# Optimization experiments

Measured on AMD Instinct MI355X. Metric: run time of the kernel, lower is better.

## Reference

```python
import jax, jax.numpy as jnp
import numpy as np

N_HEAD = 12


def setup_inputs() -> dict:
    key = jax.random.key(0)
    k1, k2, k3 = jax.random.split(key, 3)
    B, S, D = 4, 2048, 768
    x = jax.random.normal(k1, (B, S, D), dtype=jnp.float32)
    std = 0.02
    w_attn = jax.random.normal(k2, (D, 3 * D), dtype=jnp.float32) * std
    b_attn = jnp.zeros((3 * D,), dtype=jnp.float32)
    w_proj = jax.random.normal(k3, (D, D), dtype=jnp.float32) * std
    b_proj = jnp.zeros((D,), dtype=jnp.float32)
    return {"x": x, "w_attn": w_attn, "b_attn": b_attn,
            "w_proj": w_proj, "b_proj": b_proj}


def reference(x, w_attn, b_attn, w_proj, b_proj):
    B, S, D = x.shape
    H = N_HEAD
    hd = D // H
    # c_attn: [B,S,3D]
    qkv = jnp.einsum('bsd,de->bse', x, w_attn) + b_attn
    q, k, v = jnp.split(qkv, 3, axis=2)
    # split heads -> [B,H,S,hd]
    q = q.reshape(B, S, H, hd).transpose(0, 2, 1, 3)
    k = k.reshape(B, S, H, hd).transpose(0, 2, 1, 3)
    v = v.reshape(B, S, H, hd).transpose(0, 2, 1, 3)
    # scores [B,H,S,S]; scale=False in original default
    w = jnp.einsum('bhqd,bhkd->bhqk', q, k)
    # original mask trick: w*b + 1e-9*(1-b), b = lower-triangular ones
    mask = jnp.tril(jnp.ones((S, S), dtype=w.dtype))
    w = w * mask + 1e-9 * (1 - mask)
    w = jax.nn.softmax(w, axis=-1)
    a = jnp.einsum('bhqk,bhkd->bhqd', w, v)
    # merge heads -> [B,S,D]
    a = a.transpose(0, 2, 1, 3).reshape(B, S, D)
    # c_proj
    out = jnp.einsum('bsd,de->bse', a, w_proj) + b_proj
    return out
```

## Files before the change

kernel.cpp:

```cpp
#include <hip/hip_runtime.h>
#include <cstdint>

typedef unsigned short u16;
typedef __bf16 bf16;
typedef bf16 bf16x8 __attribute__((ext_vector_type(8)));
typedef u16 u16x4 __attribute__((ext_vector_type(4)));
typedef u16 u16x8 __attribute__((ext_vector_type(8)));
typedef float f32x4 __attribute__((ext_vector_type(4)));

__device__ __forceinline__ u16 f2b(float f) {
    return __builtin_bit_cast(u16, (bf16)f);
}
__device__ __forceinline__ float b2f(u16 u) {
    return __uint_as_float(((unsigned)u) << 16);
}
__device__ __forceinline__ float ex2(float x) {
#if __has_builtin(__builtin_amdgcn_exp2f)
    return __builtin_amdgcn_exp2f(x);
#else
    return exp2f(x);
#endif
}
__device__ __forceinline__ void load_lds16(const void* g, void* l) {
    auto gp = reinterpret_cast<const __attribute__((address_space(1))) void*>(
        reinterpret_cast<uintptr_t>(g));
    auto lp = reinterpret_cast<__attribute__((address_space(3))) void*>(
        reinterpret_cast<uintptr_t>(l));
    __builtin_amdgcn_global_load_lds(gp, lp, 16, 0, 0);
}
__device__ __forceinline__ f32x4 mfma16(bf16x8 a, bf16x8 b, f32x4 c) {
    return __builtin_amdgcn_mfma_f32_16x16x32_bf16(a, b, c, 0, 0, 0);
}

#define LOG2E 1.44269504088896340736f

__global__ __launch_bounds__(256) void prep_kernel(const float* __restrict__ x,
                                                   u16* __restrict__ xb,
                                                   const float* __restrict__ wa,
                                                   const float* __restrict__ wp,
                                                   u16* __restrict__ wTa,
                                                   u16* __restrict__ wTp) {
    __shared__ float tile[32][33];
    const int bx = blockIdx.x;
    if (bx < 2048) {
        const int n4 = 8192 * 768 / 4;
        int i = bx * 256 + threadIdx.x;
        for (; i < n4; i += 2048 * 256) {
            float4 v = ((const float4*)x)[i];
            u16x4 r;
            r[0] = f2b(v.x); r[1] = f2b(v.y); r[2] = f2b(v.z); r[3] = f2b(v.w);
            *(u16x4*)&xb[(size_t)i * 4] = r;
        }
        return;
    }
    const int idx = bx - 2048;
    const int nx = idx % 96, ky = idx / 96;
    const float* w;
    u16* wT;
    int N, n0;
    if (nx < 72) { w = wa; wT = wTa; N = 2304; n0 = nx * 32; }
    else         { w = wp; wT = wTp; N = 768;  n0 = (nx - 72) * 32; }
    const int K = 768, k0 = ky * 32;
    const int tx = threadIdx.x & 31, ty = threadIdx.x >> 5;
#pragma unroll
    for (int i = 0; i < 4; ++i)
        tile[ty + i * 8][tx] = w[(size_t)(k0 + ty + i * 8) * N + n0 + tx];
    __syncthreads();
#pragma unroll
    for (int i = 0; i < 4; ++i)
        wT[(size_t)(n0 + ty + i * 8) * K + k0 + tx] = f2b(tile[tx][ty + i * 8]);
}

template <int MODE>
__global__ __launch_bounds__(256, 2) void gemm_kernel(const u16* __restrict__ A,
                                                      const u16* __restrict__ Bt,
                                                      const float* __restrict__ bias,
                                                      void* __restrict__ out,
                                                      u16* __restrict__ vt,
                                                      float* __restrict__ ts_raw,
                                                      int M, int N, int K) {
    __shared__ __align__(16) u16 SMEM[4 * 128 * 64];
    const int tid = threadIdx.x;
    const int wave = tid >> 6, lane = tid & 63;
    const int l15 = lane & 15, lg = lane >> 4;
    const int gx = gridDim.x;
    const int nwg = gx * gridDim.y;
    const int lin = blockIdx.y * gx + blockIdx.x;
    const int swz = (lin & 7) * (nwg >> 3) + (lin >> 3);
    const int tm = (swz / gx) * 128, tn = (swz % gx) * 128;
    const int wr = (wave >> 1) * 64, wc = (wave & 1) * 64;

    f32x4 acc[4][4] = {};

    const int rbase = wave * 8 + (lane >> 3);
    const int sslot = (lane & 7) ^ (rbase & 7);
    const u16* gA = A + (size_t)(tm + rbase) * K + sslot * 8;
    const u16* gB = Bt + (size_t)(tn + rbase) * K + sslot * 8;
    const int woff = wave * 8 * 64;
    const int nkt = K >> 6;

#pragma unroll
    for (int i = 0; i < 4; ++i) {
        load_lds16(gA + (size_t)i * 32 * K, SMEM + woff + i * 32 * 64);
        load_lds16(gB + (size_t)i * 32 * K, SMEM + 8192 + woff + i * 32 * 64);
    }

    for (int kt = 0; kt < nkt; ++kt) {
        __syncthreads();
        const int cur = kt & 1;
        if (kt + 1 < nkt) {
            u16* ldsA = SMEM + (cur ^ 1) * 2 * 8192 + woff;
            u16* ldsB = ldsA + 8192;
#pragma unroll
            for (int i = 0; i < 4; ++i) {
                load_lds16(gA + (size_t)i * 32 * K + (kt + 1) * 64, ldsA + i * 32 * 64);
                load_lds16(gB + (size_t)i * 32 * K + (kt + 1) * 64, ldsB + i * 32 * 64);
            }
        }
        const u16* As = SMEM + cur * 2 * 8192;
        const u16* Bs = As + 8192;
#pragma unroll
        for (int kk = 0; kk < 64; kk += 32) {
            const int sb = kk >> 3;
            bf16x8 af[4], bfr[4];
#pragma unroll
            for (int m = 0; m < 4; ++m) {
                int row = wr + m * 16 + l15;
                af[m] = *(const bf16x8*)&As[row * 64 + (((sb + lg) ^ (row & 7))) * 8];
            }
#pragma unroll
            for (int n = 0; n < 4; ++n) {
                int row = wc + n * 16 + l15;
                bfr[n] = *(const bf16x8*)&Bs[row * 64 + (((sb + lg) ^ (row & 7))) * 8];
            }
#pragma unroll
            for (int m = 0; m < 4; ++m)
#pragma unroll
                for (int n = 0; n < 4; ++n)
                    acc[m][n] = mfma16(bfr[n], af[m], acc[m][n]);
        }
    }

    if (MODE == 1 && tn >= 1536) {
        const int b = tm >> 11;
        const int s0 = (tm & 2047) + wr;
        const int st = s0 >> 6;
        const int hh = (tn + wc - 1536) >> 6;
        const int bh = b * 12 + hh;
        f32x4 colsum[4] = {};
#pragma unroll
        for (int m = 0; m < 4; ++m) {
            const int s = s0 + m * 16 + l15;
#pragma unroll
            for (int n = 0; n < 4; ++n) {
                const int col = tn + wc + n * 16 + lg * 4;
                f32x4 v = acc[m][n] + *(const f32x4*)&bias[col];
                colsum[n] += v;
                const int dl = n * 16 + lg * 4;
#pragma unroll
                for (int r = 0; r < 4; ++r)
                    vt[((size_t)bh * 64 + dl + r) * 2048 + s] = f2b(v[r]);
            }
        }
#pragma unroll
        for (int n = 0; n < 4; ++n)
#pragma unroll
            for (int off = 1; off < 16; off <<= 1) {
                colsum[n][0] += __shfl_xor(colsum[n][0], off);
                colsum[n][1] += __shfl_xor(colsum[n][1], off);
                colsum[n][2] += __shfl_xor(colsum[n][2], off);
                colsum[n][3] += __shfl_xor(colsum[n][3], off);
            }
        if (l15 == 0) {
#pragma unroll
            for (int n = 0; n < 4; ++n)
                *(f32x4*)&ts_raw[((size_t)bh * 32 + st) * 64 + n * 16 + lg * 4] =
                    colsum[n];
        }
        return;
    }

    const float sc = (MODE == 1 && tn < 768) ? LOG2E : 1.f;
#pragma unroll
    for (int m = 0; m < 4; ++m) {
        const size_t row = (size_t)(tm + wr + m * 16 + l15);
#pragma unroll
        for (int n = 0; n < 4; ++n) {
            const int col = tn + wc + n * 16 + lg * 4;
            f32x4 v = (acc[m][n] + *(const f32x4*)&bias[col]) * sc;
            if constexpr (MODE == 1) {
                u16x4 pk;
#pragma unroll
                for (int r = 0; r < 4; ++r) pk[r] = f2b(v[r]);
                *(u16x4*)&((u16*)out)[row * N + col] = pk;
            } else {
                *(f32x4*)&((float*)out)[row * N + col] = v;
            }
        }
    }
}

__global__ __launch_bounds__(256, 5) void attn_kernel(const u16* __restrict__ qkv,
                                                      const u16* __restrict__ vt,
                                                      const float* __restrict__ ts_raw,
                                                      u16* __restrict__ aout) {
    __shared__ __align__(16) u16 Ks[2][64 * 64];
    __shared__ __align__(16) u16 Vs[2][64 * 64];
    const int bh = blockIdx.x;
    const int qt = 31 - blockIdx.y;
    const int b = bh / 12, h = bh % 12;
    const int tid = threadIdx.x, wave = tid >> 6, lane = tid & 63;
    const int l15 = lane & 15, lg = lane >> 4;
    const int q0 = qt * 64 + wave * 16;
    const size_t rowbase = (size_t)b * 2048;
    const float MASKVAL = 1e-9f * LOG2E;
    const float THR2 = 8.0f * LOG2E;

    bf16x8 qf[2];
#pragma unroll
    for (int ks = 0; ks < 2; ++ks)
        qf[ks] = *(const bf16x8*)(qkv + (rowbase + q0 + l15) * 2304 + h * 64 +
                                  ks * 32 + lg * 8);

    f32x4 o[4] = {};
    float mrun = -1e30f;
    f32x4 lacc = {};

    const int rbase = wave * 8 + (lane >> 3);
    const int sslot = (lane & 7) ^ (rbase & 7);
    const int sig0 = ((rbase & 0x1C) << 1) | (rbase & 3);
    const u16* gK = qkv + (rowbase + sig0) * 2304 + 768 + h * 64 + sslot * 8;
    const u16* gV = vt + ((size_t)bh * 64 + rbase) * 2048 + sslot * 8;
    const int ldsoff = wave * 8 * 64;
    u16* sK0 = &Ks[0][ldsoff];
    u16* sK1 = &Ks[1][ldsoff];
    u16* sV0 = &Vs[0][ldsoff];
    u16* sV1 = &Vs[1][ldsoff];
    const int xk0 = ((0 + lg) ^ (l15 & 7)) * 8;
    const int xk1 = ((4 + lg) ^ (l15 & 7)) * 8;

#define STAGE_PAIR(Kd, Vd, kp, vp)                       \
    load_lds16(kp, Kd);                                  \
    load_lds16(kp + (size_t)4 * 2304, Kd + 32 * 64);     \
    load_lds16(vp, Vd);                                  \
    load_lds16(vp + (size_t)32 * 2048, Vd + 32 * 64);

    auto process = [&](const u16* Kb, const u16* Vb, int kt) {
        f32x4 sacc[4] = {};
        __builtin_amdgcn_s_setprio(1);
#pragma unroll
        for (int n = 0; n < 4; ++n) {
            const int ra = (n * 16 + l15) * 64;
            sacc[n] = mfma16(*(const bf16x8*)&Kb[ra + xk0], qf[0], sacc[n]);
            sacc[n] = mfma16(*(const bf16x8*)&Kb[ra + xk1], qf[1], sacc[n]);
        }
        __builtin_amdgcn_s_setprio(0);

        if (kt == qt) {
            const int q = q0 + l15;
            const int kb = kt * 64 + lg * 8;
#pragma unroll
            for (int n = 0; n < 4; ++n) {
                const int kn = kb + (n & 1) * 32 + ((n >> 1) << 2);
#pragma unroll
                for (int r = 0; r < 4; ++r)
                    if (kn + r > q) sacc[n][r] = MASKVAL;
            }
        }

        float mx = fmaxf(fmaxf(sacc[0][0], sacc[0][1]), fmaxf(sacc[0][2], sacc[0][3]));
#pragma unroll
        for (int n = 1; n < 4; ++n)
            mx = fmaxf(mx, fmaxf(fmaxf(sacc[n][0], sacc[n][1]),
                                 fmaxf(sacc[n][2], sacc[n][3])));
        if (__any(mx > mrun + THR2)) {
            float rm = fmaxf(mx, __shfl_xor(mx, 16));
            rm = fmaxf(rm, __shfl_xor(rm, 32));
            const float mnew = fmaxf(mrun, rm);
            const float alpha = ex2(mrun - mnew);
            mrun = mnew;
            lacc *= alpha;
#pragma unroll
            for (int dn = 0; dn < 4; ++dn) o[dn] *= alpha;
        }

#pragma unroll
        for (int n = 0; n < 4; ++n)
#pragma unroll
            for (int r = 0; r < 4; ++r)
                sacc[n][r] = ex2(sacc[n][r] - mrun);
        lacc += (sacc[0] + sacc[1]) + (sacc[2] + sacc[3]);

        bf16x8 bp0, bp1;
#pragma unroll
        for (int j = 0; j < 4; ++j) {
            bp0[j]     = (bf16)sacc[0][j];
            bp0[j + 4] = (bf16)sacc[2][j];
            bp1[j]     = (bf16)sacc[1][j];
            bp1[j + 4] = (bf16)sacc[3][j];
        }

        __builtin_amdgcn_s_setprio(1);
#pragma unroll
        for (int dn = 0; dn < 4; ++dn) {
            const int ra = (dn * 16 + l15) * 64;
            o[dn] = mfma16(*(const bf16x8*)&Vb[ra + xk0], bp0, o[dn]);
            o[dn] = mfma16(*(const bf16x8*)&Vb[ra + xk1], bp1, o[dn]);
        }
        __builtin_amdgcn_s_setprio(0);
    };

    const int nkt = qt + 1;
    STAGE_PAIR(sK0, sV0, gK, gV);
    const u16* gKp = gK + (size_t)64 * 2304;
    const u16* gVp = gV + 64;

    int kt = 0;
    for (;;) {
        __syncthreads();
        if (kt + 1 < nkt) {
            STAGE_PAIR(sK1, sV1, gKp, gVp);
            gKp += (size_t)64 * 2304; gVp += 64;
        }
        process(Ks[0], Vs[0], kt);
        if (++kt == nkt) break;
        __syncthreads();
        if (kt + 1 < nkt) {
            STAGE_PAIR(sK0, sV0, gKp, gVp);
            gKp += (size_t)64 * 2304; gVp += 64;
        }
        process(Ks[1], Vs[1], kt);
        if (++kt == nkt) break;
    }
#undef STAGE_PAIR

    float lrun = (lacc[0] + lacc[1]) + (lacc[2] + lacc[3]);
    lrun += __shfl_xor(lrun, 16);
    lrun += __shfl_xor(lrun, 32);

    if (qt < 31) {
        const float nf = (float)((31 - qt) * 64);
        const float mnew = fmaxf(mrun, MASKVAL);
        const float a = ex2(mrun - mnew);
        const float c = ex2(MASKVAL - mnew);
        lrun = lrun * a + nf * c;
        f32x4 suf[4] = {};
        for (int t = qt + 1; t < 32; ++t) {
            const float* sp = ts_raw + ((size_t)bh * 32 + t) * 64;
#pragma unroll
            for (int dn = 0; dn < 4; ++dn)
                suf[dn] += *(const f32x4*)&sp[dn * 16 + lg * 4];
        }
#pragma unroll
        for (int dn = 0; dn < 4; ++dn)
            o[dn] = o[dn] * a + suf[dn] * c;
    }

    const float inv = 1.f / lrun;
    const size_t row = rowbase + q0 + l15;
#pragma unroll
    for (int dn = 0; dn < 4; ++dn) {
        u16x4 st;
#pragma unroll
        for (int r = 0; r < 4; ++r) st[r] = f2b(o[dn][r] * inv);
        *(u16x4*)&aout[row * 768 + h * 64 + dn * 16 + lg * 4] = st;
    }
}

extern "C" void kernel_launch(void* const* d_in, const int* in_sizes, int n_in,
                              void* d_out, int out_size, void* d_ws, size_t ws_size,
                              hipStream_t stream) {
    const float* x      = (const float*)d_in[0];
    const float* w_attn = (const float*)d_in[1];
    const float* b_attn = (const float*)d_in[2];
    const float* w_proj = (const float*)d_in[3];
    const float* b_proj = (const float*)d_in[4];
    float* out = (float*)d_out;
    char* ws = (char*)d_ws;

    u16* xb       = (u16*)(ws + 0);
    u16* wTa      = (u16*)(ws + 12582912);
    u16* wTp      = (u16*)(ws + 16121856);
    u16* qkv      = (u16*)(ws + 17301504);
    u16* vt       = (u16*)(ws + 55050240);
    float* ts_raw = (float*)(ws + 67633152);
    u16* aout     = (u16*)(ws + 0);

    prep_kernel<<<dim3(2048 + 2304), dim3(256), 0, stream>>>(x, xb, w_attn, w_proj,
                                                             wTa, wTp);
    gemm_kernel<1><<<dim3(18, 64), dim3(256), 0, stream>>>(xb, wTa, b_attn,
                                                           (void*)qkv, vt, ts_raw,
                                                           8192, 2304, 768);
    attn_kernel<<<dim3(48, 32), dim3(256), 0, stream>>>(qkv, vt, ts_raw, aout);
    gemm_kernel<0><<<dim3(6, 64), dim3(256), 0, stream>>>(aout, wTp, b_proj,
                                                          (void*)out, nullptr, nullptr,
                                                          8192, 768, 768);
}
```

Measured before the change: 199.0 us.

## Process 128 query rows per attention block, two m-tiles per wave

Doubles the attention query tile from 64 to 128 rows, so each wave now handles two 16-row MFMA tiles. Every K and V fragment read from LDS feeds two MFMAs, which halves LDS traffic and global K/V staging per query row. The grid is halved, diagonal masking now covers the last two key tiles, and launch bounds drop from 5 to 4 waves per SIMD to make room for the extra accumulators. The trade-off is fewer, longer blocks with coarser causal load imbalance, plus higher register pressure.

Measured after the change: 243.6 us. 22.4% more time.

```diff
diff --git a/kernel.cpp b/kernel.cpp
--- a/kernel.cpp
+++ b/kernel.cpp
@@ -200,31 +200,33 @@
     }
 }
 
-__global__ __launch_bounds__(256, 5) void attn_kernel(const u16* __restrict__ qkv,
+__global__ __launch_bounds__(256, 4) void attn_kernel(const u16* __restrict__ qkv,
                                                       const u16* __restrict__ vt,
                                                       const float* __restrict__ ts_raw,
                                                       u16* __restrict__ aout) {
     __shared__ __align__(16) u16 Ks[2][64 * 64];
     __shared__ __align__(16) u16 Vs[2][64 * 64];
     const int bh = blockIdx.x;
-    const int qt = 31 - blockIdx.y;
+    const int qt = 15 - blockIdx.y;
     const int b = bh / 12, h = bh % 12;
     const int tid = threadIdx.x, wave = tid >> 6, lane = tid & 63;
     const int l15 = lane & 15, lg = lane >> 4;
-    const int q0 = qt * 64 + wave * 16;
+    const int q0 = qt * 128 + wave * 32;
     const size_t rowbase = (size_t)b * 2048;
     const float MASKVAL = 1e-9f * LOG2E;
     const float THR2 = 8.0f * LOG2E;
 
-    bf16x8 qf[2];
-#pragma unroll
-    for (int ks = 0; ks < 2; ++ks)
-        qf[ks] = *(const bf16x8*)(qkv + (rowbase + q0 + l15) * 2304 + h * 64 +
-                                  ks * 32 + lg * 8);
-
-    f32x4 o[4] = {};
+    bf16x8 qf[2][2];
+#pragma unroll
+    for (int m = 0; m < 2; ++m)
+#pragma unroll
+        for (int ks = 0; ks < 2; ++ks)
+            qf[m][ks] = *(const bf16x8*)(qkv + (rowbase + q0 + m * 16 + l15) * 2304 +
+                                         h * 64 + ks * 32 + lg * 8);
+
+    f32x4 o[2][4] = {};
     float mrun = -1e30f;
-    f32x4 lacc = {};
+    f32x4 lacc[2] = {};
 
     const int rbase = wave * 8 + (lane >> 3);
     const int sslot = (lane & 7) ^ (rbase & 7);
@@ -246,71 +248,94 @@
     load_lds16(vp + (size_t)32 * 2048, Vd + 32 * 64);
 
     auto process = [&](const u16* Kb, const u16* Vb, int kt) {
-        f32x4 sacc[4] = {};
+        f32x4 s0[4] = {}, s1[4] = {};
         __builtin_amdgcn_s_setprio(1);
 #pragma unroll
         for (int n = 0; n < 4; ++n) {
             const int ra = (n * 16 + l15) * 64;
-            sacc[n] = mfma16(*(const bf16x8*)&Kb[ra + xk0], qf[0], sacc[n]);
-            sacc[n] = mfma16(*(const bf16x8*)&Kb[ra + xk1], qf[1], sacc[n]);
+            bf16x8 a0 = *(const bf16x8*)&Kb[ra + xk0];
+            bf16x8 a1 = *(const bf16x8*)&Kb[ra + xk1];
+            s0[n] = mfma16(a0, qf[0][0], s0[n]);
+            s1[n] = mfma16(a0, qf[1][0], s1[n]);
+            s0[n] = mfma16(a1, qf[0][1], s0[n]);
+            s1[n] = mfma16(a1, qf[1][1], s1[n]);
         }
         __builtin_amdgcn_s_setprio(0);
 
-        if (kt == qt) {
-            const int q = q0 + l15;
+        if (kt >= 2 * qt) {
             const int kb = kt * 64 + lg * 8;
 #pragma unroll
             for (int n = 0; n < 4; ++n) {
                 const int kn = kb + (n & 1) * 32 + ((n >> 1) << 2);
 #pragma unroll
-                for (int r = 0; r < 4; ++r)
-                    if (kn + r > q) sacc[n][r] = MASKVAL;
-            }
-        }
-
-        float mx = fmaxf(fmaxf(sacc[0][0], sacc[0][1]), fmaxf(sacc[0][2], sacc[0][3]));
+                for (int r = 0; r < 4; ++r) {
+                    if (kn + r > q0 + l15)      s0[n][r] = MASKVAL;
+                    if (kn + r > q0 + 16 + l15) s1[n][r] = MASKVAL;
+                }
+            }
+        }
+
+        float mx = fmaxf(fmaxf(s0[0][0], s0[0][1]), fmaxf(s0[0][2], s0[0][3]));
 #pragma unroll
         for (int n = 1; n < 4; ++n)
-            mx = fmaxf(mx, fmaxf(fmaxf(sacc[n][0], sacc[n][1]),
-                                 fmaxf(sacc[n][2], sacc[n][3])));
+            mx = fmaxf(mx, fmaxf(fmaxf(s0[n][0], s0[n][1]),
+                                 fmaxf(s0[n][2], s0[n][3])));
+#pragma unroll
+        for (int n = 0; n < 4; ++n)
+            mx = fmaxf(mx, fmaxf(fmaxf(s1[n][0], s1[n][1]),
+                                 fmaxf(s1[n][2], s1[n][3])));
         if (__any(mx > mrun + THR2)) {
             float rm = fmaxf(mx, __shfl_xor(mx, 16));
             rm = fmaxf(rm, __shfl_xor(rm, 32));
             const float mnew = fmaxf(mrun, rm);
             const float alpha = ex2(mrun - mnew);
             mrun = mnew;
-            lacc *= alpha;
-#pragma unroll
-            for (int dn = 0; dn < 4; ++dn) o[dn] *= alpha;
+            lacc[0] *= alpha;
+            lacc[1] *= alpha;
+#pragma unroll
+            for (int m = 0; m < 2; ++m)
+#pragma unroll
+                for (int dn = 0; dn < 4; ++dn) o[m][dn] *= alpha;
         }
 
 #pragma unroll
         for (int n = 0; n < 4; ++n)
 #pragma unroll
-            for (int r = 0; r < 4; ++r)
-                sacc[n][r] = ex2(sacc[n][r] - mrun);
-        lacc += (sacc[0] + sacc[1]) + (sacc[2] + sacc[3]);
-
-        bf16x8 bp0, bp1;
+            for (int r = 0; r < 4; ++r) {
+                s0[n][r] = ex2(s0[n][r] - mrun);
+                s1[n][r] = ex2(s1[n][r] - mrun);
+            }
+        lacc[0] += (s0[0] + s0[1]) + (s0[2] + s0[3]);
+        lacc[1] += (s1[0] + s1[1]) + (s1[2] + s1[3]);
+
+        bf16x8 bp00, bp01, bp10, bp11;
 #pragma unroll
         for (int j = 0; j < 4; ++j) {
-            bp0[j]     = (bf16)sacc[0][j];
-            bp0[j + 4] = (bf16)sacc[2][j];
-            bp1[j]     = (bf16)sacc[1][j];
-            bp1[j + 4] = (bf16)sacc[3][j];
+            bp00[j]     = (bf16)s0[0][j];
+            bp00[j + 4] = (bf16)s0[2][j];
+            bp01[j]     = (bf16)s0[1][j];
+            bp01[j + 4] = (bf16)s0[3][j];
+            bp10[j]     = (bf16)s1[0][j];
+            bp10[j + 4] = (bf16)s1[2][j];
+            bp11[j]     = (bf16)s1[1][j];
+            bp11[j + 4] = (bf16)s1[3][j];
         }
 
         __builtin_amdgcn_s_setprio(1);
 #pragma unroll
         for (int dn = 0; dn < 4; ++dn) {
             const int ra = (dn * 16 + l15) * 64;
-            o[dn] = mfma16(*(const bf16x8*)&Vb[ra + xk0], bp0, o[dn]);
-            o[dn] = mfma16(*(const bf16x8*)&Vb[ra + xk1], bp1, o[dn]);
+            bf16x8 v0 = *(const bf16x8*)&Vb[ra + xk0];
+            bf16x8 v1 = *(const bf16x8*)&Vb[ra + xk1];
+            o[0][dn] = mfma16(v0, bp00, o[0][dn]);
+            o[1][dn] = mfma16(v0, bp10, o[1][dn]);
+            o[0][dn] = mfma16(v1, bp01, o[0][dn]);
+            o[1][dn] = mfma16(v1, bp11, o[1][dn]);
         }
         __builtin_amdgcn_s_setprio(0);
     };
 
-    const int nkt = qt + 1;
+    const int nkt = 2 * qt + 2;
     STAGE_PAIR(sK0, sV0, gK, gV);
     const u16* gKp = gK + (size_t)64 * 2304;
     const u16* gVp = gV + 64;
@@ -334,36 +359,47 @@
     }
 #undef STAGE_PAIR
 
-    float lrun = (lacc[0] + lacc[1]) + (lacc[2] + lacc[3]);
-    lrun += __shfl_xor(lrun, 16);
-    lrun += __shfl_xor(lrun, 32);
-
-    if (qt < 31) {
-        const float nf = (float)((31 - qt) * 64);
+    float lrun[2];
+#pragma unroll
+    for (int m = 0; m < 2; ++m) {
+        float lr = (lacc[m][0] + lacc[m][1]) + (lacc[m][2] + lacc[m][3]);
+        lr += __shfl_xor(lr, 16);
+        lr += __shfl_xor(lr, 32);
+        lrun[m] = lr;
+    }
+
+    if (qt < 15) {
+        const float nf = (float)((15 - qt) * 128);
         const float mnew = fmaxf(mrun, MASKVAL);
         const float a = ex2(mrun - mnew);
         const float c = ex2(MASKVAL - mnew);
-        lrun = lrun * a + nf * c;
+        lrun[0] = lrun[0] * a + nf * c;
+        lrun[1] = lrun[1] * a + nf * c;
         f32x4 suf[4] = {};
-        for (int t = qt + 1; t < 32; ++t) {
+        for (int t = 2 * qt + 2; t < 32; ++t) {
             const float* sp = ts_raw + ((size_t)bh * 32 + t) * 64;
 #pragma unroll
             for (int dn = 0; dn < 4; ++dn)
                 suf[dn] += *(const f32x4*)&sp[dn * 16 + lg * 4];
         }
 #pragma unroll
-        for (int dn = 0; dn < 4; ++dn)
-            o[dn] = o[dn] * a + suf[dn] * c;
-    }
-
-    const float inv = 1.f / lrun;
-    const size_t row = rowbase + q0 + l15;
-#pragma unroll
-    for (int dn = 0; dn < 4; ++dn) {
-        u16x4 st;
-#pragma unroll
-        for (int r = 0; r < 4; ++r) st[r] = f2b(o[dn][r] * inv);
-        *(u16x4*)&aout[row * 768 + h * 64 + dn * 16 + lg * 4] = st;
+        for (int m = 0; m < 2; ++m)
+#pragma unroll
+            for (int dn = 0; dn < 4; ++dn)
+                o[m][dn] = o[m][dn] * a + suf[dn] * c;
+    }
+
+#pragma unroll
+    for (int m = 0; m < 2; ++m) {
+        const float inv = 1.f / lrun[m];
+        const size_t row = rowbase + q0 + m * 16 + l15;
+#pragma unroll
+        for (int dn = 0; dn < 4; ++dn) {
+            u16x4 st;
+#pragma unroll
+            for (int r = 0; r < 4; ++r) st[r] = f2b(o[m][dn][r] * inv);
+            *(u16x4*)&aout[row * 768 + h * 64 + dn * 16 + lg * 4] = st;
+        }
     }
 }
 
@@ -391,7 +427,7 @@
     gemm_kernel<1><<<dim3(18, 64), dim3(256), 0, stream>>>(xb, wTa, b_attn,
                                                            (void*)qkv, vt, ts_raw,
                                                            8192, 2304, 768);
-    attn_kernel<<<dim3(48, 32), dim3(256), 0, stream>>>(qkv, vt, ts_raw, aout);
+    attn_kernel<<<dim3(48, 16), dim3(256), 0, stream>>>(qkv, vt, ts_raw, aout);
     gemm_kernel<0><<<dim3(6, 64), dim3(256), 0, stream>>>(aout, wTp, b_proj,
                                                           (void*)out, nullptr, nullptr,
                                                           8192, 768, 768);
```
